# Kernel optimization log

Measured on AMD Instinct MI355X. Metric: run time of the kernel, lower is better.

The kernel has to match this reference:

```python
import jax, jax.numpy as jnp
import numpy as np

C = 256
CK = C // 8  # key/query channels


def setup_inputs() -> dict:
    key = jax.random.key(0)
    ks = jax.random.split(key, 7)
    B, H, W = 8, 64, 64
    x = jax.random.normal(ks[0], (B, C, H, W), dtype=jnp.float32)
    # 1x1 conv weights (out_ch, in_ch) and biases. Spectral norm is a weight
    # reparameterization; at forward time it is just a conv with (normalized)
    # weights, so we sample weights directly.
    Wf = jax.random.normal(ks[1], (CK, C), dtype=jnp.float32) * 0.02
    bf = jnp.zeros((CK,), dtype=jnp.float32)
    Wg = jax.random.normal(ks[2], (CK, C), dtype=jnp.float32) * 0.02
    bg = jnp.zeros((CK,), dtype=jnp.float32)
    Wh = jax.random.normal(ks[3], (C, C), dtype=jnp.float32) * 0.02
    bh = jnp.zeros((C,), dtype=jnp.float32)
    gamma = jnp.ones((1,), dtype=jnp.float32) * 0.5  # nonzero so attention path matters
    return {"x": x, "Wf": Wf, "bf": bf, "Wg": Wg, "bg": bg, "Wh": Wh, "bh": bh, "gamma": gamma}


def reference(x, Wf, bf, Wg, bg, Wh, bh, gamma):
    b, c, h, w = x.shape
    n = h * w
    xf = x.reshape(b, c, n)  # [B, C, N]
    # 1x1 convs == per-pixel linear maps
    fx = jnp.einsum("kc,bcn->bkn", Wf, xf) + bf[None, :, None]  # [B, CK, N]
    gx = jnp.einsum("kc,bcn->bkn", Wg, xf) + bg[None, :, None]  # [B, CK, N]
    hx = jnp.einsum("oc,bcn->bon", Wh, xf) + bh[None, :, None]  # [B, C, N]
    # sx[b, i, j] = <fx[:, i], gx[:, j]>
    sx = jnp.einsum("bki,bkj->bij", fx, gx)  # [B, N, N]
    # torch F.softmax(sx, dim=1): normalize over the first N axis (i)
    beta = jax.nn.softmax(sx, axis=1)
    ox = jnp.einsum("bci,bij->bcj", hx, beta).reshape(b, c, h, w)
    return gamma.reshape(()) * ox + x
```

## Files before the change

### kernel.cpp

```cpp
#include <hip/hip_runtime.h>
#include <stdint.h>


typedef __bf16 bf16;
typedef __bf16 bf16x8 __attribute__((ext_vector_type(8)));
typedef float  f32x16 __attribute__((ext_vector_type(16)));
typedef float  f32x4  __attribute__((ext_vector_type(4)));

#define BATCH 8
#define CC    256
#define CKK   32
#define NN    4096
#define LOG2E 1.4426950408889634f

__device__ __forceinline__ f32x16 zero16() {
  f32x16 z;
#pragma unroll
  for (int i = 0; i < 16; ++i) z[i] = 0.0f;
  return z;
}

__device__ __forceinline__ unsigned pack2(float lo, float hi) {
  unsigned short a = __builtin_bit_cast(unsigned short, (bf16)lo);
  unsigned short b = __builtin_bit_cast(unsigned short, (bf16)hi);
  return (unsigned)a | ((unsigned)b << 16);
}

__device__ __forceinline__ f32x16 mfma32(bf16x8 a, bf16x8 b, f32x16 c) {
  return __builtin_amdgcn_mfma_f32_32x32x16_bf16(a, b, c, 0, 0, 0);
}

#define GLDS16(srcp, dstp)                                                         \
  __builtin_amdgcn_global_load_lds(                                               \
      (const __attribute__((address_space(1))) void*)(srcp),                      \
      (__attribute__((address_space(3))) void*)(dstp), 16, 0, 0)

__global__ __launch_bounds__(256) void k_transpose(const float* __restrict__ x,
                                                   bf16* __restrict__ xT) {
  __shared__ float tile[64][65];
  const int n0 = blockIdx.x * 64;
  const int c0 = blockIdx.y * 64;
  const int b  = blockIdx.z;
  const int t = threadIdx.x;
  const int tn = t & 63, trow = t >> 6;
#pragma unroll
  for (int i = 0; i < 16; ++i) {
    int c = trow + i * 4;
    tile[c][tn] = x[((size_t)(b * CC + c0 + c)) * NN + n0 + tn];
  }
  __syncthreads();
#pragma unroll
  for (int i = 0; i < 16; ++i) {
    int n = trow + i * 4;
    xT[((size_t)(b * NN + n0 + n)) * CC + c0 + tn] = (bf16)tile[tn][n];
  }
}

__global__ __launch_bounds__(64) void k_wprep(const float* __restrict__ Wf, const float* __restrict__ bfv,
                                              const float* __restrict__ Wg, const float* __restrict__ bg,
                                              const float* __restrict__ Wh, const float* __restrict__ bh,
                                              bf16* __restrict__ Wcat, float* __restrict__ bcat) {
  const int ko = blockIdx.x;
  const int t = threadIdx.x;
  const float* src;
  float scale = 1.0f;
  if (ko < 32) src = Wf + (size_t)ko * CC;
  else if (ko < 64) { src = Wg + (size_t)(ko - 32) * CC; scale = LOG2E; }
  else src = Wh + (size_t)(ko - 64) * CC;
#pragma unroll
  for (int i = 0; i < 4; ++i)
    Wcat[(size_t)ko * CC + t + i * 64] = (bf16)(src[t + i * 64] * scale);
  if (ko == 0) {
    for (int i = t; i < 320; i += 64) {
      float v = (i < 32) ? bfv[i] : (i < 64) ? bg[i - 32] * LOG2E : bh[i - 64];
      bcat[i] = v;
    }
  }
}

__global__ __launch_bounds__(256, 1) void k_proj(const bf16* __restrict__ xT,
                                                 const bf16* __restrict__ Wcat,
                                                 const float* __restrict__ bcat,
                                                 bf16* __restrict__ fxT, bf16* __restrict__ gxT,
                                                 bf16* __restrict__ hx) {
  const int d = blockIdx.x;
  const int b = d & 7, nb = d >> 3;
  const int t = threadIdx.x;
  const int w = t >> 6, ln = t & 63, ln31 = ln & 31, h = ln >> 5;
  const int n = nb * 128 + w * 32 + ln31;

  f32x16 acc[10];
#pragma unroll
  for (int mt = 0; mt < 10; ++mt) acc[mt] = zero16();

  const bf16* xrow = xT + ((size_t)(b * NN + n)) * CC;
#pragma unroll
  for (int ks = 0; ks < 16; ++ks) {
    bf16x8 bfrag = *(const bf16x8*)(xrow + ks * 16 + h * 8);
#pragma unroll
    for (int mt = 0; mt < 10; ++mt) {
      bf16x8 afrag = *(const bf16x8*)(Wcat + (size_t)(mt * 32 + ln31) * CC + ks * 16 + h * 8);
      acc[mt] = mfma32(afrag, bfrag, acc[mt]);
    }
  }

#pragma unroll
  for (int mt = 0; mt < 10; ++mt) {
#pragma unroll
    for (int q = 0; q < 4; ++q) {
      const int ko0 = mt * 32 + 8 * q + 4 * h;
      float v0 = acc[mt][4 * q + 0] + bcat[ko0 + 0];
      float v1 = acc[mt][4 * q + 1] + bcat[ko0 + 1];
      float v2 = acc[mt][4 * q + 2] + bcat[ko0 + 2];
      float v3 = acc[mt][4 * q + 3] + bcat[ko0 + 3];
      if (mt < 2) {
        bf16* dst = (mt == 0 ? fxT : gxT) + ((size_t)(b * NN + n)) * CKK + (8 * q + 4 * h);
        uint2 pv;
        pv.x = pack2(v0, v1);
        pv.y = pack2(v2, v3);
        *(uint2*)dst = pv;
      } else {
        const int c = ko0 - 64;
        hx[((size_t)(b * CC + c + 0)) * NN + n] = (bf16)v0;
        hx[((size_t)(b * CC + c + 1)) * NN + n] = (bf16)v1;
        hx[((size_t)(b * CC + c + 2)) * NN + n] = (bf16)v2;
        hx[((size_t)(b * CC + c + 3)) * NN + n] = (bf16)v3;
      }
    }
  }
}

__global__ __launch_bounds__(512, 2) void k_attn(const bf16* __restrict__ fxT,
                                                 const bf16* __restrict__ gxT,
                                                 const bf16* __restrict__ hx,
                                                 const float* __restrict__ x,
                                                 const float* __restrict__ gammap,
                                                 float* __restrict__ out) {
  extern __shared__ __align__(16) char smem[];
  __shared__ float lsh[128];
  const int d = blockIdx.x;
  const int b = d & 7, jb = d >> 3;
  const int t = threadIdx.x;
  const int g = t >> 8;
  const int tg = t & 255;
  const int wg = tg >> 6;
  const int ln = t & 63, ln31 = ln & 31, h = ln >> 5;
  const int j = jb * 128 + wg * 32 + ln31;
  const int kbase = g * 2048;

  const bf16* fxb = fxT + (size_t)b * NN * CKK;
  const bf16* hxb = hx + (size_t)b * CC * NN;

  bf16* vsg = (bf16*)smem + g * 32768;
  bf16* ksg = (bf16*)(smem + 131072) + g * 4096;

  const bf16* qrow = gxT + ((size_t)b * NN + j) * CKK;
  bf16x8 qf0 = *(const bf16x8*)(qrow + h * 8);
  bf16x8 qf1 = *(const bf16x8*)(qrow + 16 + h * 8);
  asm volatile("" ::: "memory");

  const int tau = (ln31 >> 1) & 3;
  const int vo0 = ln31 * 32 + ((h ^ tau) * 8);
  const int vo1 = ln31 * 32 + (((2 + h) ^ tau) * 8);

  const int lrow = ln >> 2;
  const int lcol = ((ln & 3) ^ ((ln >> 3) & 3)) * 8;
  const bf16* vlane = hxb + (size_t)(wg * 64 + lrow) * NN + lcol;
  const bf16* klane = fxb + (size_t)(wg * 16 + lrow) * CKK + lcol;

#define STAGE(sidx, i0s)                                                      \
  {                                                                            \
    _Pragma("unroll")                                                          \
    for (int q = 0; q < 4; ++q)                                                \
      GLDS16(vlane + (size_t)q * 16 * NN + (i0s),                              \
             vsg + (sidx) * 8192 + (wg * 64 + q * 16) * 32);                   \
    if (wg < 2)                                                                \
      GLDS16(klane + (size_t)(i0s) * CKK, ksg + (sidx) * 1024 + wg * 512);     \
  }

  f32x16 oacc[8];
#pragma unroll
  for (int ct = 0; ct < 8; ++ct) oacc[ct] = zero16();
  float l_run = 0.0f;

  STAGE(0, kbase);
  STAGE(1, kbase + 32);
  if (wg < 2) { asm volatile("s_waitcnt vmcnt(5)" ::: "memory"); }
  else        { asm volatile("s_waitcnt vmcnt(4)" ::: "memory"); }
  __builtin_amdgcn_s_barrier();
  asm volatile("" ::: "memory");

  f32x16 s_cur = zero16();
  {
    const bf16* kt = ksg;
    bf16x8 kf0 = *(const bf16x8*)(kt + vo0);
    bf16x8 kf1 = *(const bf16x8*)(kt + vo1);
    s_cur = mfma32(kf0, qf0, s_cur);
    s_cur = mfma32(kf1, qf1, s_cur);
  }

#pragma unroll 2
  for (int kb = 0; kb < 64; ++kb) {
    STAGE((kb + 2) & 3, kbase + ((kb + 2) & 63) * 32);

    if (wg < 2) { asm volatile("s_waitcnt vmcnt(5)" ::: "memory"); }
    else        { asm volatile("s_waitcnt vmcnt(4)" ::: "memory"); }
    __builtin_amdgcn_s_barrier();
    asm volatile("" ::: "memory");

    f32x16 s_next = zero16();
    {
      const bf16* kt = ksg + ((kb + 1) & 3) * 1024;
      bf16x8 kf0 = *(const bf16x8*)(kt + vo0);
      bf16x8 kf1 = *(const bf16x8*)(kt + vo1);
      s_next = mfma32(kf0, qf0, s_next);
      s_next = mfma32(kf1, qf1, s_next);
    }

    float ls0 = 0.0f, ls1 = 0.0f;
    unsigned pk[4][2];
#pragma unroll
    for (int q = 0; q < 4; ++q)
#pragma unroll
      for (int wi = 0; wi < 2; ++wi) {
        float a0 = __builtin_exp2f(s_cur[4 * q + 2 * wi]);
        float a1 = __builtin_exp2f(s_cur[4 * q + 2 * wi + 1]);
        ls0 += a0; ls1 += a1;
        pk[q][wi] = pack2(a0, a1);
      }
    float lsum = ls0 + ls1;
    lsum += __shfl_xor(lsum, 32);
    l_run += lsum;

    bf16x8 pf[2];
#pragma unroll
    for (int ks = 0; ks < 2; ++ks) {
      const int qb = 2 * ks;
      union { unsigned u[4]; bf16x8 v; } pu;
#pragma unroll
      for (int wi = 0; wi < 2; ++wi) {
        unsigned a  = pk[qb][wi];
        unsigned bv = pk[qb + 1][wi];
        unsigned sv = h ? a : bv;
        unsigned rv = (unsigned)__shfl_xor((int)sv, 32);
        pu.u[wi]     = h ? rv : a;
        pu.u[2 + wi] = h ? bv : rv;
      }
      pf[ks] = pu.v;
    }

    const bf16* vb = vsg + (kb & 3) * 8192;
    __builtin_amdgcn_s_setprio(1);
#pragma unroll
    for (int ct = 0; ct < 8; ++ct) {
      const bf16* vrow = vb + ct * 1024;
      oacc[ct] = mfma32(*(const bf16x8*)(vrow + vo0), pf[0], oacc[ct]);
      oacc[ct] = mfma32(*(const bf16x8*)(vrow + vo1), pf[1], oacc[ct]);
    }
    __builtin_amdgcn_s_setprio(0);

    s_cur = s_next;
  }

  asm volatile("s_waitcnt vmcnt(0) lgkmcnt(0)" ::: "memory");
  __builtin_amdgcn_s_barrier();
  asm volatile("" ::: "memory");

  float* obuf = (float*)smem;
  const int jl = wg * 32 + ln31;
  if (g == 1) {
#pragma unroll
    for (int ct = 0; ct < 8; ++ct)
#pragma unroll
      for (int q = 0; q < 4; ++q) {
        f32x4 v;
        v[0] = oacc[ct][4 * q + 0];
        v[1] = oacc[ct][4 * q + 1];
        v[2] = oacc[ct][4 * q + 2];
        v[3] = oacc[ct][4 * q + 3];
        *(f32x4*)&obuf[jl * 260 + ct * 32 + 8 * q + 4 * h] = v;
      }
    if (h == 0) lsh[jl] = l_run;
  }
  __syncthreads();
  if (g == 0) {
    const float l = l_run + lsh[jl];
    const float ginv = gammap[0] / l;
    const float* xb = x + (size_t)b * CC * NN;
    float* ob = out + (size_t)b * CC * NN;
#pragma unroll
    for (int ct = 0; ct < 8; ++ct)
#pragma unroll
      for (int q = 0; q < 4; ++q) {
        f32x4 vB = *(const f32x4*)&obuf[jl * 260 + ct * 32 + 8 * q + 4 * h];
#pragma unroll
        for (int s = 0; s < 4; ++s) {
          int c = ct * 32 + 8 * q + 4 * h + s;
          size_t idx = (size_t)c * NN + j;
          float val = oacc[ct][4 * q + s] + vB[s];
          ob[idx] = fmaf(ginv, val, xb[idx]);
        }
      }
  }
#undef STAGE
}

extern "C" void kernel_launch(void* const* d_in, const int* in_sizes, int n_in,
                              void* d_out, int out_size, void* d_ws, size_t ws_size,
                              hipStream_t stream) {
  const float* x     = (const float*)d_in[0];
  const float* Wf    = (const float*)d_in[1];
  const float* bfv   = (const float*)d_in[2];
  const float* Wg    = (const float*)d_in[3];
  const float* bg    = (const float*)d_in[4];
  const float* Wh    = (const float*)d_in[5];
  const float* bh    = (const float*)d_in[6];
  const float* gamma = (const float*)d_in[7];
  float* out = (float*)d_out;

  char* ws = (char*)d_ws;
  bf16* fxT  = (bf16*)(ws);
  bf16* gxT  = (bf16*)(ws + 2097152);
  bf16* hx   = (bf16*)(ws + 4194304);
  bf16* Wcat = (bf16*)(ws + 20971520);
  float* bcat = (float*)(ws + 21135360);
  bf16* xT = (bf16*)d_out;

  k_transpose<<<dim3(64, 4, 8), 256, 0, stream>>>(x, xT);
  k_wprep<<<dim3(320), 64, 0, stream>>>(Wf, bfv, Wg, bg, Wh, bh, Wcat, bcat);
  k_proj<<<dim3(256), 256, 0, stream>>>(xT, Wcat, bcat, fxT, gxT, hx);
  k_attn<<<dim3(256), 512, 147456, stream>>>(fxT, gxT, hx, x, gamma, out);
}
```

Measured before the change: 145.1 us.

## Stagger softmax and PV across wave groups, use permlane32 swap for P packing

```diff
diff --git a/kernel.cpp b/kernel.cpp
--- a/kernel.cpp
+++ b/kernel.cpp
@@ -3,6 +3,7 @@
 
 
 typedef __bf16 bf16;
+typedef __bf16 bf16x2 __attribute__((ext_vector_type(2)));
 typedef __bf16 bf16x8 __attribute__((ext_vector_type(8)));
 typedef float  f32x16 __attribute__((ext_vector_type(16)));
 typedef float  f32x4  __attribute__((ext_vector_type(4)));
@@ -21,9 +22,8 @@
 }
 
 __device__ __forceinline__ unsigned pack2(float lo, float hi) {
-  unsigned short a = __builtin_bit_cast(unsigned short, (bf16)lo);
-  unsigned short b = __builtin_bit_cast(unsigned short, (bf16)hi);
-  return (unsigned)a | ((unsigned)b << 16);
+  bf16x2 v = {(bf16)lo, (bf16)hi};
+  return __builtin_bit_cast(unsigned, v);
 }
 
 __device__ __forceinline__ f32x16 mfma32(bf16x8 a, bf16x8 b, f32x16 c) {
@@ -168,12 +168,15 @@
   const bf16* vlane = hxb + (size_t)(wg * 64 + lrow) * NN + lcol;
   const bf16* klane = fxb + (size_t)(wg * 16 + lrow) * CKK + lcol;
 
-#define STAGE(sidx, i0s)                                                      \
+#define STAGEV(sidx, i0s)                                                     \
   {                                                                            \
     _Pragma("unroll")                                                          \
     for (int q = 0; q < 4; ++q)                                                \
       GLDS16(vlane + (size_t)q * 16 * NN + (i0s),                              \
              vsg + (sidx) * 8192 + (wg * 64 + q * 16) * 32);                   \
+  }
+#define STAGEK(sidx, i0s)                                                     \
+  {                                                                            \
     if (wg < 2)                                                                \
       GLDS16(klane + (size_t)(i0s) * CKK, ksg + (sidx) * 1024 + wg * 512);     \
   }
@@ -183,84 +186,86 @@
   for (int ct = 0; ct < 8; ++ct) oacc[ct] = zero16();
   float l_run = 0.0f;
 
-  STAGE(0, kbase);
-  STAGE(1, kbase + 32);
-  if (wg < 2) { asm volatile("s_waitcnt vmcnt(5)" ::: "memory"); }
-  else        { asm volatile("s_waitcnt vmcnt(4)" ::: "memory"); }
+  auto QK = [&](int slot) -> f32x16 {
+    const bf16* kt = ksg + slot * 1024;
+    bf16x8 kf0 = *(const bf16x8*)(kt + vo0);
+    bf16x8 kf1 = *(const bf16x8*)(kt + vo1);
+    f32x16 s = zero16();
+    s = mfma32(kf0, qf0, s);
+    s = mfma32(kf1, qf1, s);
+    return s;
+  };
+  auto SM = [&](const f32x16& s, bf16x8* pf) {
+    float ls0 = 0.0f, ls1 = 0.0f;
+    unsigned pk[4][2];
+#pragma unroll
+    for (int q = 0; q < 4; ++q)
+#pragma unroll
+      for (int wi = 0; wi < 2; ++wi) {
+        float a0 = __builtin_exp2f(s[4 * q + 2 * wi]);
+        float a1 = __builtin_exp2f(s[4 * q + 2 * wi + 1]);
+        ls0 += a0; ls1 += a1;
+        pk[q][wi] = pack2(a0, a1);
+      }
+    float lsum = ls0 + ls1;
+    lsum += __shfl_xor(lsum, 32);
+    l_run += lsum;
+#pragma unroll
+    for (int ks = 0; ks < 2; ++ks) {
+      union { unsigned u[4]; bf16x8 v; } pu;
+#pragma unroll
+      for (int wi = 0; wi < 2; ++wi) {
+        unsigned xx = pk[2 * ks][wi];
+        unsigned yy = pk[2 * ks + 1][wi];
+        asm("v_permlane32_swap_b32 %0, %1" : "+v"(xx), "+v"(yy));
+        pu.u[wi]     = xx;
+        pu.u[2 + wi] = yy;
+      }
+      pf[ks] = pu.v;
+    }
+  };
+  auto PV = [&](const bf16x8* pf, int slot) {
+    const bf16* vb = vsg + slot * 8192;
+    __builtin_amdgcn_s_setprio(1);
+#pragma unroll
+    for (int ct = 0; ct < 8; ++ct) {
+      const bf16* vrow = vb + ct * 1024;
+      oacc[ct] = mfma32(*(const bf16x8*)(vrow + vo0), pf[0], oacc[ct]);
+      oacc[ct] = mfma32(*(const bf16x8*)(vrow + vo1), pf[1], oacc[ct]);
+    }
+    __builtin_amdgcn_s_setprio(0);
+  };
+
+  STAGEV(0, kbase); STAGEK(0, kbase);
+  STAGEV(1, kbase + 32); STAGEK(1, kbase + 32);
+  STAGEK(2, kbase + 64);
+  asm volatile("s_waitcnt vmcnt(0)" ::: "memory");
   __builtin_amdgcn_s_barrier();
   asm volatile("" ::: "memory");
 
-  f32x16 s_cur = zero16();
-  {
-    const bf16* kt = ksg;
-    bf16x8 kf0 = *(const bf16x8*)(kt + vo0);
-    bf16x8 kf1 = *(const bf16x8*)(kt + vo1);
-    s_cur = mfma32(kf0, qf0, s_cur);
-    s_cur = mfma32(kf1, qf1, s_cur);
-  }
-
-#pragma unroll 2
+  f32x16 s_cur = QK(0);
+  bf16x8 pfs[2];
+  bf16x8 pft[2];
+
   for (int kb = 0; kb < 64; ++kb) {
-    STAGE((kb + 2) & 3, kbase + ((kb + 2) & 63) * 32);
-
     if (wg < 2) { asm volatile("s_waitcnt vmcnt(5)" ::: "memory"); }
     else        { asm volatile("s_waitcnt vmcnt(4)" ::: "memory"); }
     __builtin_amdgcn_s_barrier();
     asm volatile("" ::: "memory");
 
-    f32x16 s_next = zero16();
-    {
-      const bf16* kt = ksg + ((kb + 1) & 3) * 1024;
-      bf16x8 kf0 = *(const bf16x8*)(kt + vo0);
-      bf16x8 kf1 = *(const bf16x8*)(kt + vo1);
-      s_next = mfma32(kf0, qf0, s_next);
-      s_next = mfma32(kf1, qf1, s_next);
-    }
-
-    float ls0 = 0.0f, ls1 = 0.0f;
-    unsigned pk[4][2];
-#pragma unroll
-    for (int q = 0; q < 4; ++q)
-#pragma unroll
-      for (int wi = 0; wi < 2; ++wi) {
-        float a0 = __builtin_exp2f(s_cur[4 * q + 2 * wi]);
-        float a1 = __builtin_exp2f(s_cur[4 * q + 2 * wi + 1]);
-        ls0 += a0; ls1 += a1;
-        pk[q][wi] = pack2(a0, a1);
-      }
-    float lsum = ls0 + ls1;
-    lsum += __shfl_xor(lsum, 32);
-    l_run += lsum;
-
-    bf16x8 pf[2];
-#pragma unroll
-    for (int ks = 0; ks < 2; ++ks) {
-      const int qb = 2 * ks;
-      union { unsigned u[4]; bf16x8 v; } pu;
-#pragma unroll
-      for (int wi = 0; wi < 2; ++wi) {
-        unsigned a  = pk[qb][wi];
-        unsigned bv = pk[qb + 1][wi];
-        unsigned sv = h ? a : bv;
-        unsigned rv = (unsigned)__shfl_xor((int)sv, 32);
-        pu.u[wi]     = h ? rv : a;
-        pu.u[2 + wi] = h ? bv : rv;
-      }
-      pf[ks] = pu.v;
-    }
-
-    const bf16* vb = vsg + (kb & 3) * 8192;
-    __builtin_amdgcn_s_setprio(1);
-#pragma unroll
-    for (int ct = 0; ct < 8; ++ct) {
-      const bf16* vrow = vb + ct * 1024;
-      oacc[ct] = mfma32(*(const bf16x8*)(vrow + vo0), pf[0], oacc[ct]);
-      oacc[ct] = mfma32(*(const bf16x8*)(vrow + vo1), pf[1], oacc[ct]);
-    }
-    __builtin_amdgcn_s_setprio(0);
-
-    s_cur = s_next;
-  }
+    STAGEV((kb + 2) & 3, kbase + ((kb + 2) & 63) * 32);
+    STAGEK((kb + 3) & 3, kbase + ((kb + 3) & 63) * 32);
+
+    if (g == 0) {
+      SM(s_cur, pft);
+      PV(pft, kb & 3);
+    } else {
+      if (kb > 0) PV(pfs, (kb - 1) & 3);
+      SM(s_cur, pfs);
+    }
+    s_cur = QK((kb + 1) & 3);
+  }
+  if (g == 1) PV(pfs, 63 & 3);
 
   asm volatile("s_waitcnt vmcnt(0) lgkmcnt(0)" ::: "memory");
   __builtin_amdgcn_s_barrier();
@@ -302,7 +307,8 @@
         }
       }
   }
-#undef STAGE
+#undef STAGEV
+#undef STAGEK
 }
 
 extern "C" void kernel_launch(void* const* d_in, const int* in_sizes, int n_in,
```

Result: slower. 150.8 us (+3.9%).
